# Optimization experiments

Measured on AMD Instinct MI355X. Metric: run time of the kernel, lower is better.

## Reference

```python
import jax, jax.numpy as jnp
import numpy as np

N_NODES = 100000
N_EDGES = 800000
D_R = 128   # node feature dim
D_H = 96    # edge message dim
D_OUT = 96  # output Linear out_features (bias removed per remove_bias)


def setup_inputs() -> dict:
    key = jax.random.key(0)
    k_r, k_h, k_nbr, k_w = jax.random.split(key, 4)
    r = jax.random.normal(k_r, (N_NODES, D_R), dtype=jnp.float32)
    h = jax.random.normal(k_h, (N_EDGES, D_H), dtype=jnp.float32)
    nbrs = jax.random.randint(k_nbr, (N_EDGES, 2), 0, N_NODES, dtype=jnp.int64)
    # Linear(D_R + D_H -> D_OUT, bias=False); torch Linear weight is [out, in]
    W_out = jax.random.normal(k_w, (D_OUT, D_R + D_H), dtype=jnp.float32) * (1.0 / np.sqrt(D_R + D_H))
    return {"r": r, "h": h, "nbrs": nbrs, "W_out": W_out}


def reference(r, h, nbrs, W_out):
    num_nodes = r.shape[0]
    # chemprop_msg_to_node: scatter-sum directed-edge messages onto destination node nbrs[:, 0]
    msg_to_node = jax.ops.segment_sum(h, nbrs[:, 0], num_segments=num_nodes)  # [N, D_H]
    cat_node = jnp.concatenate((r, msg_to_node), axis=1)                      # [N, D_R + D_H]
    new_node_feats = jax.nn.relu(cat_node @ W_out.T)                          # [N, D_OUT]
    return new_node_feats
```

## Files before the change

### kernel.cpp

```cpp
#include <hip/hip_runtime.h>
#include <hip/hip_bf16.h>

#define D_R 128
#define D_H 96
#define D_IN 224
#define D_OUT 96
#define CAP 64
#define NW 21504

typedef __attribute__((ext_vector_type(8))) short short8;
typedef __attribute__((ext_vector_type(4))) float f32x4;

static __device__ inline unsigned short f2b(float x) {
    __hip_bfloat16 b = __float2bfloat16(x);
    unsigned short u;
    __builtin_memcpy(&u, &b, 2);
    return u;
}

__global__ __launch_bounds__(256) void init_kernel(
    int* __restrict__ deg, int n_nodes,
    const float* __restrict__ W, unsigned short* __restrict__ W16)
{
    int i = blockIdx.x * 256 + threadIdx.x;
    if (i < n_nodes) deg[i] = 0;
    if (i < NW) W16[i] = f2b(W[i]);
}

__global__ __launch_bounds__(256) void build_kernel(
    const int* __restrict__ nbrs, int* __restrict__ deg,
    int* __restrict__ bucket, int n_edges)
{
    int k = blockIdx.x * 256 + threadIdx.x;
    int e0 = 2 * k;
    if (e0 >= n_edges) return;
    if (e0 + 1 < n_edges) {
        int4 q = *reinterpret_cast<const int4*>(nbrs + 2 * e0);
        int p0 = atomicAdd(&deg[q.x], 1);
        if (p0 < CAP) bucket[(size_t)q.x * CAP + p0] = e0;
        int p1 = atomicAdd(&deg[q.z], 1);
        if (p1 < CAP) bucket[(size_t)q.z * CAP + p1] = e0 + 1;
    } else {
        int d = nbrs[2 * e0];
        int p0 = atomicAdd(&deg[d], 1);
        if (p0 < CAP) bucket[(size_t)d * CAP + p0] = e0;
    }
}

__global__ __launch_bounds__(256) void gather_kernel(
    const float* __restrict__ h, const int* __restrict__ deg_arr,
    const int* __restrict__ bucket, unsigned short* __restrict__ msg16,
    int n_nodes)
{
    int t = blockIdx.x * 256 + threadIdx.x;
    int node = t / 24;
    if (node >= n_nodes) return;
    int f4 = (t - node * 24) * 4;
    int deg = deg_arr[node]; if (deg > CAP) deg = CAP;
    const int* brow = bucket + (size_t)node * CAP;

    f32x4 a0 = (f32x4){0.f,0.f,0.f,0.f}, a1 = a0, a2 = a0, a3 = a0;
    int i = 0;
    for (; i + 4 <= deg; i += 4) {
        int4 e = *reinterpret_cast<const int4*>(brow + i);
        a0 += __builtin_nontemporal_load(
            reinterpret_cast<const f32x4*>(h + (size_t)e.x * D_H + f4));
        a1 += __builtin_nontemporal_load(
            reinterpret_cast<const f32x4*>(h + (size_t)e.y * D_H + f4));
        a2 += __builtin_nontemporal_load(
            reinterpret_cast<const f32x4*>(h + (size_t)e.z * D_H + f4));
        a3 += __builtin_nontemporal_load(
            reinterpret_cast<const f32x4*>(h + (size_t)e.w * D_H + f4));
    }
    for (; i < deg; ++i) {
        int e = brow[i];
        a0 += __builtin_nontemporal_load(
            reinterpret_cast<const f32x4*>(h + (size_t)e * D_H + f4));
    }
    f32x4 s = (a0 + a1) + (a2 + a3);
    ushort4 o;
    o.x = f2b(s.x); o.y = f2b(s.y); o.z = f2b(s.z); o.w = f2b(s.w);
    *reinterpret_cast<ushort4*>(msg16 + (size_t)node * D_H + f4) = o;
}

__global__ __launch_bounds__(256) void mfma_gemm_kernel(
    const float* __restrict__ r, const unsigned short* __restrict__ msg16,
    const unsigned short* __restrict__ W16, float* __restrict__ out, int n_nodes)
{
    const int lane = threadIdx.x & 63;
    const int wv   = threadIdx.x >> 6;
    const int cl   = lane & 15;
    const int kch  = (lane >> 4) * 8;

    const int rowbase = blockIdx.x * 128 + wv * 32;

    f32x4 acc[2][6];
#pragma unroll
    for (int mf = 0; mf < 2; ++mf)
#pragma unroll
        for (int nf = 0; nf < 6; ++nf) acc[mf][nf] = (f32x4){0.f, 0.f, 0.f, 0.f};

    int arow0 = rowbase + cl;       if (arow0 >= n_nodes) arow0 = n_nodes - 1;
    int arow1 = rowbase + 16 + cl;  if (arow1 >= n_nodes) arow1 = n_nodes - 1;

    const float* rb[2] = { r + (size_t)arow0 * D_R + kch,
                           r + (size_t)arow1 * D_R + kch };
    const unsigned short* mb[2] = { msg16 + (size_t)arow0 * D_H + kch,
                                    msg16 + (size_t)arow1 * D_H + kch };
    const unsigned short* wb = W16 + (size_t)cl * D_IN + kch;

#pragma unroll
    for (int ks = 0; ks < 4; ++ks) {
        const int k0 = ks * 32;
        short8 a[2];
#pragma unroll
        for (int mf = 0; mf < 2; ++mf) {
            const f32x4 u = __builtin_nontemporal_load(
                reinterpret_cast<const f32x4*>(rb[mf] + k0));
            const f32x4 v = __builtin_nontemporal_load(
                reinterpret_cast<const f32x4*>(rb[mf] + k0 + 4));
            short8 tv;
            tv[0] = (short)f2b(u.x); tv[1] = (short)f2b(u.y);
            tv[2] = (short)f2b(u.z); tv[3] = (short)f2b(u.w);
            tv[4] = (short)f2b(v.x); tv[5] = (short)f2b(v.y);
            tv[6] = (short)f2b(v.z); tv[7] = (short)f2b(v.w);
            a[mf] = tv;
        }
#pragma unroll
        for (int nf = 0; nf < 6; ++nf) {
            const short8 b = *reinterpret_cast<const short8*>(
                wb + (size_t)nf * 16 * D_IN + k0);
            acc[0][nf] = __builtin_amdgcn_mfma_f32_16x16x32_bf16(a[0], b, acc[0][nf], 0, 0, 0);
            acc[1][nf] = __builtin_amdgcn_mfma_f32_16x16x32_bf16(a[1], b, acc[1][nf], 0, 0, 0);
        }
    }

#pragma unroll
    for (int ks = 0; ks < 3; ++ks) {
        const int k0 = ks * 32;
        short8 a[2];
        a[0] = *reinterpret_cast<const short8*>(mb[0] + k0);
        a[1] = *reinterpret_cast<const short8*>(mb[1] + k0);
#pragma unroll
        for (int nf = 0; nf < 6; ++nf) {
            const short8 b = *reinterpret_cast<const short8*>(
                wb + (size_t)nf * 16 * D_IN + D_R + k0);
            acc[0][nf] = __builtin_amdgcn_mfma_f32_16x16x32_bf16(a[0], b, acc[0][nf], 0, 0, 0);
            acc[1][nf] = __builtin_amdgcn_mfma_f32_16x16x32_bf16(a[1], b, acc[1][nf], 0, 0, 0);
        }
    }

    const int g4 = (lane >> 4) * 4;
#pragma unroll
    for (int mf = 0; mf < 2; ++mf) {
#pragma unroll
        for (int q = 0; q < 4; ++q) {
            const int row = rowbase + mf * 16 + g4 + q;
            if (row < n_nodes) {
                float* op = out + (size_t)row * D_OUT + cl;
#pragma unroll
                for (int nf = 0; nf < 6; ++nf)
                    __builtin_nontemporal_store(fmaxf(acc[mf][nf][q], 0.f), op + nf * 16);
            }
        }
    }
}

extern "C" void kernel_launch(void* const* d_in, const int* in_sizes, int n_in,
                              void* d_out, int out_size, void* d_ws, size_t ws_size,
                              hipStream_t stream) {
    const float* r    = (const float*)d_in[0];
    const float* h    = (const float*)d_in[1];
    const int*   nbrs = (const int*)d_in[2];
    const float* W    = (const float*)d_in[3];
    float*       out  = (float*)d_out;

    const int n_nodes = in_sizes[0] / D_R;
    const int n_edges = in_sizes[2] / 2;

    char* ws = (char*)d_ws;
    unsigned short* msg16 = (unsigned short*)ws;
    size_t off = (size_t)n_nodes * D_H * sizeof(unsigned short);
    int* deg    = (int*)(ws + off);  off += (size_t)n_nodes * sizeof(int);
    int* bucket = (int*)(ws + off);  off += (size_t)n_nodes * CAP * sizeof(int);
    unsigned short* W16 = (unsigned short*)(ws + off);

    const int pair_blocks = ((n_edges + 1) / 2 + 255) / 256;
    const int init_blocks = (n_nodes > NW ? n_nodes : NW) / 256 + 1;

    init_kernel<<<init_blocks, 256, 0, stream>>>(deg, n_nodes, W, W16);
    build_kernel<<<pair_blocks, 256, 0, stream>>>(nbrs, deg, bucket, n_edges);

    {
        long long total = (long long)n_nodes * 24;
        int blocks = (int)((total + 255) / 256);
        gather_kernel<<<blocks, 256, 0, stream>>>(h, deg, bucket, msg16, n_nodes);
    }
    {
        dim3 grid((n_nodes + 127) / 128);
        mfma_gemm_kernel<<<grid, 256, 0, stream>>>(r, msg16, W16, out, n_nodes);
    }
}
```

Before: 164.4 us.

## Sort nodes by degree for gather balance and stage weights in LDS

```diff
diff --git a/kernel.cpp b/kernel.cpp
--- a/kernel.cpp
+++ b/kernel.cpp
@@ -5,8 +5,10 @@
 #define D_H 96
 #define D_IN 224
 #define D_OUT 96
-#define CAP 64
+#define CAP 48
+#define NBIN (CAP + 1)
 #define NW 21504
+#define WPAD 232
 
 typedef __attribute__((ext_vector_type(8))) short short8;
 typedef __attribute__((ext_vector_type(4))) float f32x4;
@@ -20,11 +22,13 @@
 
 __global__ __launch_bounds__(256) void init_kernel(
     int* __restrict__ deg, int n_nodes,
-    const float* __restrict__ W, unsigned short* __restrict__ W16)
+    const float* __restrict__ W, unsigned short* __restrict__ W16,
+    int* __restrict__ gbin)
 {
     int i = blockIdx.x * 256 + threadIdx.x;
     if (i < n_nodes) deg[i] = 0;
     if (i < NW) W16[i] = f2b(W[i]);
+    if (i < 2 * NBIN) gbin[i] = 0;
 }
 
 __global__ __launch_bounds__(256) void build_kernel(
@@ -47,15 +51,61 @@
     }
 }
 
+__global__ __launch_bounds__(256) void bin_kernel(
+    const int* __restrict__ deg, int* __restrict__ gbin, int n)
+{
+    __shared__ int lc[NBIN];
+    if (threadIdx.x < NBIN) lc[threadIdx.x] = 0;
+    __syncthreads();
+    int i = blockIdx.x * 256 + threadIdx.x;
+    if (i < n) {
+        int d = deg[i]; if (d > CAP) d = CAP;
+        atomicAdd(&lc[d], 1);
+    }
+    __syncthreads();
+    if (threadIdx.x < NBIN && lc[threadIdx.x])
+        atomicAdd(&gbin[threadIdx.x], lc[threadIdx.x]);
+}
+
+__global__ void binscan_kernel(const int* __restrict__ gbin, int* __restrict__ cursor)
+{
+    if (threadIdx.x == 0 && blockIdx.x == 0) {
+        int run = 0;
+        for (int i = 0; i < NBIN; ++i) { cursor[i] = run; run += gbin[i]; }
+    }
+}
+
+__global__ __launch_bounds__(256) void order_kernel(
+    const int* __restrict__ deg, int* __restrict__ cursor,
+    int* __restrict__ order, int n)
+{
+    __shared__ int lcount[NBIN];
+    __shared__ int lbase[NBIN];
+    if (threadIdx.x < NBIN) lcount[threadIdx.x] = 0;
+    __syncthreads();
+    int i = blockIdx.x * 256 + threadIdx.x;
+    int myb = -1, lpos = 0;
+    if (i < n) {
+        myb = deg[i]; if (myb > CAP) myb = CAP;
+        lpos = atomicAdd(&lcount[myb], 1);
+    }
+    __syncthreads();
+    if (threadIdx.x < NBIN && lcount[threadIdx.x])
+        lbase[threadIdx.x] = atomicAdd(&cursor[threadIdx.x], lcount[threadIdx.x]);
+    __syncthreads();
+    if (myb >= 0) order[lbase[myb] + lpos] = i;
+}
+
 __global__ __launch_bounds__(256) void gather_kernel(
     const float* __restrict__ h, const int* __restrict__ deg_arr,
-    const int* __restrict__ bucket, unsigned short* __restrict__ msg16,
-    int n_nodes)
+    const int* __restrict__ bucket, const int* __restrict__ order,
+    unsigned short* __restrict__ msg16, int n_nodes)
 {
     int t = blockIdx.x * 256 + threadIdx.x;
-    int node = t / 24;
-    if (node >= n_nodes) return;
-    int f4 = (t - node * 24) * 4;
+    int g = t / 24;
+    if (g >= n_nodes) return;
+    int node = order[g];
+    int f4 = (t - g * 24) * 4;
     int deg = deg_arr[node]; if (deg > CAP) deg = CAP;
     const int* brow = bucket + (size_t)node * CAP;
 
@@ -87,6 +137,15 @@
     const float* __restrict__ r, const unsigned short* __restrict__ msg16,
     const unsigned short* __restrict__ W16, float* __restrict__ out, int n_nodes)
 {
+    __shared__ unsigned short Wl[D_OUT * WPAD];
+
+    for (int c = threadIdx.x; c < D_OUT * (D_IN / 8); c += 256) {
+        int j = c / 28, p = c - j * 28;
+        *reinterpret_cast<short8*>(&Wl[j * WPAD + p * 8]) =
+            *reinterpret_cast<const short8*>(&W16[j * D_IN + p * 8]);
+    }
+    __syncthreads();
+
     const int lane = threadIdx.x & 63;
     const int wv   = threadIdx.x >> 6;
     const int cl   = lane & 15;
@@ -107,7 +166,6 @@
                            r + (size_t)arow1 * D_R + kch };
     const unsigned short* mb[2] = { msg16 + (size_t)arow0 * D_H + kch,
                                     msg16 + (size_t)arow1 * D_H + kch };
-    const unsigned short* wb = W16 + (size_t)cl * D_IN + kch;
 
 #pragma unroll
     for (int ks = 0; ks < 4; ++ks) {
@@ -129,7 +187,7 @@
 #pragma unroll
         for (int nf = 0; nf < 6; ++nf) {
             const short8 b = *reinterpret_cast<const short8*>(
-                wb + (size_t)nf * 16 * D_IN + k0);
+                &Wl[(nf * 16 + cl) * WPAD + k0 + kch]);
             acc[0][nf] = __builtin_amdgcn_mfma_f32_16x16x32_bf16(a[0], b, acc[0][nf], 0, 0, 0);
             acc[1][nf] = __builtin_amdgcn_mfma_f32_16x16x32_bf16(a[1], b, acc[1][nf], 0, 0, 0);
         }
@@ -144,7 +202,7 @@
 #pragma unroll
         for (int nf = 0; nf < 6; ++nf) {
             const short8 b = *reinterpret_cast<const short8*>(
-                wb + (size_t)nf * 16 * D_IN + D_R + k0);
+                &Wl[(nf * 16 + cl) * WPAD + D_R + k0 + kch]);
             acc[0][nf] = __builtin_amdgcn_mfma_f32_16x16x32_bf16(a[0], b, acc[0][nf], 0, 0, 0);
             acc[1][nf] = __builtin_amdgcn_mfma_f32_16x16x32_bf16(a[1], b, acc[1][nf], 0, 0, 0);
         }
@@ -184,17 +242,25 @@
     int* deg    = (int*)(ws + off);  off += (size_t)n_nodes * sizeof(int);
     int* bucket = (int*)(ws + off);  off += (size_t)n_nodes * CAP * sizeof(int);
     unsigned short* W16 = (unsigned short*)(ws + off);
+    off += ((size_t)NW * sizeof(unsigned short) + 15) & ~(size_t)15;
+    int* gbin   = (int*)(ws + off);  off += ((size_t)NBIN * sizeof(int) + 15) & ~(size_t)15;
+    int* cursor = (int*)(ws + off);  off += ((size_t)NBIN * sizeof(int) + 15) & ~(size_t)15;
+    int* order  = (int*)(ws + off);
 
     const int pair_blocks = ((n_edges + 1) / 2 + 255) / 256;
+    const int node_blocks = (n_nodes + 255) / 256;
     const int init_blocks = (n_nodes > NW ? n_nodes : NW) / 256 + 1;
 
-    init_kernel<<<init_blocks, 256, 0, stream>>>(deg, n_nodes, W, W16);
+    init_kernel<<<init_blocks, 256, 0, stream>>>(deg, n_nodes, W, W16, gbin);
     build_kernel<<<pair_blocks, 256, 0, stream>>>(nbrs, deg, bucket, n_edges);
+    bin_kernel<<<node_blocks, 256, 0, stream>>>(deg, gbin, n_nodes);
+    binscan_kernel<<<1, 64, 0, stream>>>(gbin, cursor);
+    order_kernel<<<node_blocks, 256, 0, stream>>>(deg, cursor, order, n_nodes);
 
     {
         long long total = (long long)n_nodes * 24;
         int blocks = (int)((total + 255) / 256);
-        gather_kernel<<<blocks, 256, 0, stream>>>(h, deg, bucket, msg16, n_nodes);
+        gather_kernel<<<blocks, 256, 0, stream>>>(h, deg, bucket, order, msg16, n_nodes);
     }
     {
         dim3 grid((n_nodes + 127) / 128);
```

Result: slower. 175.1 us (+6.5%).

## Stage weights in LDS, prefetch GEMM operands, unroll gather by eight

Applied to the files above, without the earlier changes.

```diff
diff --git a/kernel.cpp b/kernel.cpp
--- a/kernel.cpp
+++ b/kernel.cpp
@@ -7,6 +7,7 @@
 #define D_OUT 96
 #define CAP 64
 #define NW 21504
+#define WPAD 232
 
 typedef __attribute__((ext_vector_type(8))) short short8;
 typedef __attribute__((ext_vector_type(4))) float f32x4;
@@ -60,24 +61,47 @@
     const int* brow = bucket + (size_t)node * CAP;
 
     f32x4 a0 = (f32x4){0.f,0.f,0.f,0.f}, a1 = a0, a2 = a0, a3 = a0;
+    f32x4 a4 = a0, a5 = a0, a6 = a0, a7 = a0;
     int i = 0;
+    for (; i + 8 <= deg; i += 8) {
+        int4 ea = *reinterpret_cast<const int4*>(brow + i);
+        int4 eb = *reinterpret_cast<const int4*>(brow + i + 4);
+        const f32x4 v0 = __builtin_nontemporal_load(
+            reinterpret_cast<const f32x4*>(h + (size_t)ea.x * D_H + f4));
+        const f32x4 v1 = __builtin_nontemporal_load(
+            reinterpret_cast<const f32x4*>(h + (size_t)ea.y * D_H + f4));
+        const f32x4 v2 = __builtin_nontemporal_load(
+            reinterpret_cast<const f32x4*>(h + (size_t)ea.z * D_H + f4));
+        const f32x4 v3 = __builtin_nontemporal_load(
+            reinterpret_cast<const f32x4*>(h + (size_t)ea.w * D_H + f4));
+        const f32x4 v4 = __builtin_nontemporal_load(
+            reinterpret_cast<const f32x4*>(h + (size_t)eb.x * D_H + f4));
+        const f32x4 v5 = __builtin_nontemporal_load(
+            reinterpret_cast<const f32x4*>(h + (size_t)eb.y * D_H + f4));
+        const f32x4 v6 = __builtin_nontemporal_load(
+            reinterpret_cast<const f32x4*>(h + (size_t)eb.z * D_H + f4));
+        const f32x4 v7 = __builtin_nontemporal_load(
+            reinterpret_cast<const f32x4*>(h + (size_t)eb.w * D_H + f4));
+        a0 += v0; a1 += v1; a2 += v2; a3 += v3;
+        a4 += v4; a5 += v5; a6 += v6; a7 += v7;
+    }
     for (; i + 4 <= deg; i += 4) {
-        int4 e = *reinterpret_cast<const int4*>(brow + i);
+        int4 ea = *reinterpret_cast<const int4*>(brow + i);
         a0 += __builtin_nontemporal_load(
-            reinterpret_cast<const f32x4*>(h + (size_t)e.x * D_H + f4));
+            reinterpret_cast<const f32x4*>(h + (size_t)ea.x * D_H + f4));
         a1 += __builtin_nontemporal_load(
-            reinterpret_cast<const f32x4*>(h + (size_t)e.y * D_H + f4));
+            reinterpret_cast<const f32x4*>(h + (size_t)ea.y * D_H + f4));
         a2 += __builtin_nontemporal_load(
-            reinterpret_cast<const f32x4*>(h + (size_t)e.z * D_H + f4));
+            reinterpret_cast<const f32x4*>(h + (size_t)ea.z * D_H + f4));
         a3 += __builtin_nontemporal_load(
-            reinterpret_cast<const f32x4*>(h + (size_t)e.w * D_H + f4));
+            reinterpret_cast<const f32x4*>(h + (size_t)ea.w * D_H + f4));
     }
     for (; i < deg; ++i) {
         int e = brow[i];
         a0 += __builtin_nontemporal_load(
             reinterpret_cast<const f32x4*>(h + (size_t)e * D_H + f4));
     }
-    f32x4 s = (a0 + a1) + (a2 + a3);
+    f32x4 s = ((a0 + a1) + (a2 + a3)) + ((a4 + a5) + (a6 + a7));
     ushort4 o;
     o.x = f2b(s.x); o.y = f2b(s.y); o.z = f2b(s.z); o.w = f2b(s.w);
     *reinterpret_cast<ushort4*>(msg16 + (size_t)node * D_H + f4) = o;
@@ -87,6 +111,8 @@
     const float* __restrict__ r, const unsigned short* __restrict__ msg16,
     const unsigned short* __restrict__ W16, float* __restrict__ out, int n_nodes)
 {
+    __shared__ unsigned short Wl[D_OUT * WPAD];
+
     const int lane = threadIdx.x & 63;
     const int wv   = threadIdx.x >> 6;
     const int cl   = lane & 15;
@@ -94,12 +120,6 @@
 
     const int rowbase = blockIdx.x * 128 + wv * 32;
 
-    f32x4 acc[2][6];
-#pragma unroll
-    for (int mf = 0; mf < 2; ++mf)
-#pragma unroll
-        for (int nf = 0; nf < 6; ++nf) acc[mf][nf] = (f32x4){0.f, 0.f, 0.f, 0.f};
-
     int arow0 = rowbase + cl;       if (arow0 >= n_nodes) arow0 = n_nodes - 1;
     int arow1 = rowbase + 16 + cl;  if (arow1 >= n_nodes) arow1 = n_nodes - 1;
 
@@ -107,7 +127,34 @@
                            r + (size_t)arow1 * D_R + kch };
     const unsigned short* mb[2] = { msg16 + (size_t)arow0 * D_H + kch,
                                     msg16 + (size_t)arow1 * D_H + kch };
-    const unsigned short* wb = W16 + (size_t)cl * D_IN + kch;
+
+    f32x4 rbuf[2][8];
+    short8 mbuf[2][3];
+#pragma unroll
+    for (int mf = 0; mf < 2; ++mf) {
+#pragma unroll
+        for (int q = 0; q < 8; ++q) {
+            const int off = (q >> 1) * 32 + (q & 1) * 4;
+            rbuf[mf][q] = __builtin_nontemporal_load(
+                reinterpret_cast<const f32x4*>(rb[mf] + off));
+        }
+#pragma unroll
+        for (int ks = 0; ks < 3; ++ks)
+            mbuf[mf][ks] = *reinterpret_cast<const short8*>(mb[mf] + ks * 32);
+    }
+
+    for (int c = threadIdx.x; c < D_OUT * (D_IN / 8); c += 256) {
+        int j = c / 28, p = c - j * 28;
+        *reinterpret_cast<short8*>(&Wl[j * WPAD + p * 8]) =
+            *reinterpret_cast<const short8*>(&W16[j * D_IN + p * 8]);
+    }
+    __syncthreads();
+
+    f32x4 acc[2][6];
+#pragma unroll
+    for (int mf = 0; mf < 2; ++mf)
+#pragma unroll
+        for (int nf = 0; nf < 6; ++nf) acc[mf][nf] = (f32x4){0.f, 0.f, 0.f, 0.f};
 
 #pragma unroll
     for (int ks = 0; ks < 4; ++ks) {
@@ -115,10 +162,8 @@
         short8 a[2];
 #pragma unroll
         for (int mf = 0; mf < 2; ++mf) {
-            const f32x4 u = __builtin_nontemporal_load(
-                reinterpret_cast<const f32x4*>(rb[mf] + k0));
-            const f32x4 v = __builtin_nontemporal_load(
-                reinterpret_cast<const f32x4*>(rb[mf] + k0 + 4));
+            const f32x4 u = rbuf[mf][2 * ks];
+            const f32x4 v = rbuf[mf][2 * ks + 1];
             short8 tv;
             tv[0] = (short)f2b(u.x); tv[1] = (short)f2b(u.y);
             tv[2] = (short)f2b(u.z); tv[3] = (short)f2b(u.w);
@@ -129,7 +174,7 @@
 #pragma unroll
         for (int nf = 0; nf < 6; ++nf) {
             const short8 b = *reinterpret_cast<const short8*>(
-                wb + (size_t)nf * 16 * D_IN + k0);
+                &Wl[(nf * 16 + cl) * WPAD + k0 + kch]);
             acc[0][nf] = __builtin_amdgcn_mfma_f32_16x16x32_bf16(a[0], b, acc[0][nf], 0, 0, 0);
             acc[1][nf] = __builtin_amdgcn_mfma_f32_16x16x32_bf16(a[1], b, acc[1][nf], 0, 0, 0);
         }
@@ -138,15 +183,12 @@
 #pragma unroll
     for (int ks = 0; ks < 3; ++ks) {
         const int k0 = ks * 32;
-        short8 a[2];
-        a[0] = *reinterpret_cast<const short8*>(mb[0] + k0);
-        a[1] = *reinterpret_cast<const short8*>(mb[1] + k0);
 #pragma unroll
         for (int nf = 0; nf < 6; ++nf) {
             const short8 b = *reinterpret_cast<const short8*>(
-                wb + (size_t)nf * 16 * D_IN + D_R + k0);
-            acc[0][nf] = __builtin_amdgcn_mfma_f32_16x16x32_bf16(a[0], b, acc[0][nf], 0, 0, 0);
-            acc[1][nf] = __builtin_amdgcn_mfma_f32_16x16x32_bf16(a[1], b, acc[1][nf], 0, 0, 0);
+                &Wl[(nf * 16 + cl) * WPAD + D_R + k0 + kch]);
+            acc[0][nf] = __builtin_amdgcn_mfma_f32_16x16x32_bf16(mbuf[0][ks], b, acc[0][nf], 0, 0, 0);
+            acc[1][nf] = __builtin_amdgcn_mfma_f32_16x16x32_bf16(mbuf[1][ks], b, acc[1][nf], 0, 0, 0);
         }
     }
 
```

New measurement: 161.0 us (median of 2 runs). -2.0%, faster.
